# Kernel optimization log

Measured on AMD Instinct MI355X. Metric: run time of the kernel, lower is better.

Reference implementation:

```python
import jax, jax.numpy as jnp
import numpy as np

EMBED = 2048
HEADS = 16
NOPE = 128      # embed // heads
VDIM = 128
ROPE = 64
Q_HEAD = NOPE + ROPE  # 192
KV_RANK = 512
BASE = 10000.0


def _rope(x, offset=0):
    # x: [b, h, n, d] with d even; rotary (lrpe_type=1) on pair-interleaved dims
    d = x.shape[-1]
    n = x.shape[-2]
    theta = BASE ** (-2.0 * jnp.arange(d // 2, dtype=jnp.float32) / d)  # [d/2]
    pos = jnp.arange(n, dtype=jnp.float32) + offset                     # [n]
    ang = pos[:, None] * theta[None, :]                                  # [n, d/2]
    cos, sin = jnp.cos(ang), jnp.sin(ang)
    x1 = x[..., 0::2]
    x2 = x[..., 1::2]
    o1 = x1 * cos - x2 * sin
    o2 = x1 * sin + x2 * cos
    return jnp.stack([o1, o2], axis=-1).reshape(x.shape)


def setup_inputs() -> dict:
    key = jax.random.key(0)
    ks = jax.random.split(key, 6)
    b, n = 2, 2048
    s = lambda fin: 1.0 / np.sqrt(fin)
    return {
        "x": jax.random.normal(ks[0], (b, n, EMBED), jnp.float32),
        "Wqa": jax.random.normal(ks[1], (EMBED, 512), jnp.float32) * s(EMBED),
        "Wqb": jax.random.normal(ks[2], (512, HEADS * Q_HEAD), jnp.float32) * s(512),
        "Wkva": jax.random.normal(ks[3], (EMBED, KV_RANK + ROPE), jnp.float32) * s(EMBED),
        "Wkvb": jax.random.normal(ks[4], (KV_RANK, HEADS * (NOPE + VDIM)), jnp.float32) * s(KV_RANK),
        "Wout": jax.random.normal(ks[5], (HEADS * VDIM, EMBED), jnp.float32) * s(HEADS * VDIM),
    }


def reference(x, Wqa, Wqb, Wkva, Wkvb, Wout):
    b, n, _ = x.shape
    # low-rank Q projection
    q = (x @ Wqa) @ Wqb                                   # [b, n, h*192]
    q = q.reshape(b, n, HEADS, Q_HEAD).transpose(0, 2, 1, 3)  # [b, h, n, 192]
    q_nope, q_pe = q[..., :NOPE], q[..., NOPE:]
    # low-rank KV compression + shared rope key
    ckv = x @ Wkva                                        # [b, n, 512+64]
    compressed, k_pe = ckv[..., :KV_RANK], ckv[..., KV_RANK:]
    k_pe = jnp.broadcast_to(k_pe[:, None], (b, HEADS, n, ROPE))
    kv = compressed @ Wkvb                                # [b, n, h*(128+128)]
    kv = kv.reshape(b, n, HEADS, NOPE + VDIM).transpose(0, 2, 1, 3)
    k_nope, v = kv[..., :NOPE], kv[..., NOPE:]
    # partial RoPE on rope slice
    q_pe = _rope(q_pe)
    k_pe = _rope(k_pe)
    qf = jnp.concatenate([q_nope, q_pe], axis=-1)         # [b, h, n, 192]
    kf = jnp.concatenate([k_nope, k_pe], axis=-1)
    # causal SDPA, scale = 1/sqrt(q_head_dim)
    scale = 1.0 / np.sqrt(Q_HEAD)
    scores = jnp.einsum("bhnd,bhmd->bhnm", qf, kf) * scale
    causal = jnp.tril(jnp.ones((n, n), dtype=bool))
    scores = jnp.where(causal, scores, jnp.finfo(scores.dtype).min)
    attn = jax.nn.softmax(scores, axis=-1)
    out = jnp.einsum("bhnm,bhmd->bhnd", attn, v)          # [b, h, n, 128]
    out = out.transpose(0, 2, 1, 3).reshape(b, n, HEADS * VDIM)
    return out @ Wout
```

## Files before the change

### kernel.cpp

```cpp
#include <hip/hip_runtime.h>
#include <math.h>

typedef __bf16 bf16;
typedef __bf16 bf16x8 __attribute__((ext_vector_type(8)));
typedef float f32x4 __attribute__((ext_vector_type(4)));

#define HEADS 16
#define QHEAD 192
#define NB 2
#define SEQ 2048
#define ROWS (NB * SEQ)
#define QSCALE2 0.10411754584f
#define CSHIFT 11.5415603272f

__global__ __launch_bounds__(256) void prep(
    const float* __restrict__ x,
    const float* __restrict__ Wqa, const float* __restrict__ Wqb,
    const float* __restrict__ Wkva, const float* __restrict__ Wkvb,
    const float* __restrict__ Wout,
    bf16* __restrict__ xb,
    bf16* __restrict__ WfT, bf16* __restrict__ WqbT,
    bf16* __restrict__ WkvbT, bf16* __restrict__ WoutT)
{
    int t = blockIdx.x;
    if (t < 8192) {
        size_t i = ((size_t)t * 256 + threadIdx.x) * 4;
        float4 v = *(const float4*)(x + i);
        xb[i]     = (bf16)v.x;
        xb[i + 1] = (bf16)v.y;
        xb[i + 2] = (bf16)v.z;
        xb[i + 3] = (bf16)v.w;
        return;
    }
    t -= 8192;
    __shared__ float tile[32][33];
    const float* in; bf16* out; int R, C;
    if (t < 1024)      {            in = Wqa;  out = WfT;                      R = 2048; C = 512;  }
    else if (t < 2176) { t -= 1024; in = Wkva; out = WfT + (size_t)512 * 2048; R = 2048; C = 576;  }
    else if (t < 3712) { t -= 2176; in = Wqb;  out = WqbT;                     R = 512;  C = 3072; }
    else if (t < 5760) { t -= 3712; in = Wkvb; out = WkvbT;                    R = 512;  C = 4096; }
    else               { t -= 5760; in = Wout; out = WoutT;                    R = 2048; C = 2048; }
    int tilesX = (C + 31) >> 5;
    int bx = (t % tilesX) * 32, by = (t / tilesX) * 32;
    int tx = threadIdx.x & 31, ty = threadIdx.x >> 5;
    for (int i = 0; i < 32; i += 8) {
        int r = by + ty + i, c = bx + tx;
        tile[ty + i][tx] = (r < R && c < C) ? in[(size_t)r * C + c] : 0.f;
    }
    __syncthreads();
    for (int i = 0; i < 32; i += 8) {
        int c = bx + ty + i, r = by + tx;
        if (c < C && r < R) out[(size_t)c * R + r] = (bf16)tile[tx][ty + i];
    }
}

#define GEMM_BODY(Aptr, LDA, Bptr, LDB, KK, BNIDX)                              \
    __shared__ bf16 As[128 * 32];                                               \
    __shared__ bf16 Bs[128 * 32];                                               \
    const int tid  = threadIdx.x;                                               \
    const int wave = tid >> 6, lane = tid & 63;                                 \
    const int quad = lane >> 4, l16 = lane & 15;                                \
    const int bm = blockIdx.x * 128, bn = (BNIDX) * 128;                        \
    const int wm = (wave >> 1) * 64, wn = (wave & 1) * 64;                      \
    const int srow = lane >> 2, scol = (lane & 3) * 8;                          \
    f32x4 acc[4][4];                                                            \
    for (int i = 0; i < 4; i++)                                                 \
        for (int j = 0; j < 4; j++)                                             \
            acc[i][j] = (f32x4){0.f, 0.f, 0.f, 0.f};                            \
    for (int k0 = 0; k0 < (KK); k0 += 32) {                                     \
        _Pragma("unroll")                                                       \
        for (int s2 = 0; s2 < 2; s2++) {                                        \
            const int seg = wave * 2 + s2;                                      \
            const bf16* ga = (Aptr) + (size_t)(bm + seg * 16 + srow) * (LDA) + k0 + scol; \
            const bf16* gb = (Bptr) + (size_t)(bn + seg * 16 + srow) * (LDB) + k0 + scol; \
            __builtin_amdgcn_global_load_lds(                                   \
                (const __attribute__((address_space(1))) void*)ga,              \
                (__attribute__((address_space(3))) void*)&As[seg * 512], 16, 0, 0); \
            __builtin_amdgcn_global_load_lds(                                   \
                (const __attribute__((address_space(1))) void*)gb,              \
                (__attribute__((address_space(3))) void*)&Bs[seg * 512], 16, 0, 0); \
        }                                                                       \
        __syncthreads();                                                        \
        bf16x8 af[4], bfv[4];                                                   \
        for (int mi = 0; mi < 4; mi++)                                          \
            af[mi] = *(const bf16x8*)&As[(wm + mi * 16 + l16) * 32 + quad * 8]; \
        for (int ni = 0; ni < 4; ni++)                                          \
            bfv[ni] = *(const bf16x8*)&Bs[(wn + ni * 16 + l16) * 32 + quad * 8];\
        for (int mi = 0; mi < 4; mi++)                                          \
            for (int ni = 0; ni < 4; ni++)                                      \
                acc[mi][ni] = __builtin_amdgcn_mfma_f32_16x16x32_bf16(          \
                    af[mi], bfv[ni], acc[mi][ni], 0, 0, 0);                     \
        __syncthreads();                                                        \
    }

template <typename OutT>
__global__ __launch_bounds__(256) void gemm_bf16(
    const bf16* __restrict__ A, int lda,
    const bf16* __restrict__ Bt, int ldb,
    OutT* __restrict__ C, int ldc,
    int N, int K)
{
    GEMM_BODY(A, lda, Bt, ldb, K, blockIdx.y)
    for (int mi = 0; mi < 4; mi++)
        for (int ni = 0; ni < 4; ni++) {
            int col = bn + wn + ni * 16 + l16;
            if (col >= N) continue;
            int row0 = bm + wm + mi * 16 + quad * 4;
            for (int r = 0; r < 4; r++)
                C[(size_t)(row0 + r) * ldc + col] = (OutT)acc[mi][ni][r];
        }
}

__global__ __launch_bounds__(256) void gemm_qkv(
    const bf16* __restrict__ tc,
    const bf16* __restrict__ WqbT, const bf16* __restrict__ WkvbT,
    bf16* __restrict__ qf, bf16* __restrict__ kf, bf16* __restrict__ kvv)
{
    const int byAll = blockIdx.y;
    const bool isQ = byAll < 24;
    const bf16* A  = isQ ? tc : tc + 512;
    const bf16* Bt = isQ ? WqbT : WkvbT;
    const int bnIdx = isQ ? byAll : byAll - 24;
    GEMM_BODY(A, 1152, Bt, 512, 512, bnIdx)
    if (isQ) {
        const bool odd = l16 & 1;
        for (int mi = 0; mi < 4; mi++)
            for (int ni = 0; ni < 4; ni++) {
                int col0 = bn + wn + ni * 16;
                int h  = col0 / 192;
                int d0 = col0 - h * 192;
                int d  = d0 + l16;
                bool roped = d0 >= 128;
                float theta = 0.f;
                if (roped) theta = powf(10000.f, -(float)((d - 128) >> 1) / 32.f);
                for (int r = 0; r < 4; r++) {
                    int row = bm + wm + mi * 16 + quad * 4 + r;
                    int b = row >> 11, n = row & 2047;
                    float v = acc[mi][ni][r], res;
                    if (roped) {
                        float p = __shfl_xor(v, 1);
                        float sn, cs;
                        sincosf((float)n * theta, &sn, &cs);
                        float x1 = odd ? p : v, x2 = odd ? v : p;
                        res = odd ? (x1 * sn + x2 * cs) : (x1 * cs - x2 * sn);
                    } else res = v;
                    qf[(((size_t)(b * HEADS + h)) * SEQ + n) * QHEAD + d] =
                        (bf16)(res * QSCALE2);
                }
            }
    } else {
        for (int mi = 0; mi < 4; mi++)
            for (int ni = 0; ni < 4; ni++) {
                int col0 = bn + wn + ni * 16;
                int h  = col0 >> 8;
                int d0 = col0 & 255;
                int d  = d0 + l16;
                for (int r = 0; r < 4; r++) {
                    int row = bm + wm + mi * 16 + quad * 4 + r;
                    int b = row >> 11, n = row & 2047;
                    bf16 v = (bf16)acc[mi][ni][r];
                    if (d0 < 128)
                        kf[(((size_t)(b * HEADS + h)) * SEQ + n) * QHEAD + d] = v;
                    else
                        kvv[(size_t)row * 2048 + h * 128 + (d - 128)] = v;
                }
            }
    }
}

__global__ __launch_bounds__(256) void rope_vt(
    const bf16* __restrict__ tc, const bf16* __restrict__ kvv,
    bf16* __restrict__ kf, bf16* __restrict__ vT)
{
    int t = blockIdx.x;
    if (t < 8192) {
        __shared__ bf16 tile[32][33];
        int bh = t >> 8, rest = t & 255;
        int dv0 = (rest >> 6) * 32, nt0 = (rest & 63) * 32;
        int b = bh >> 4, h = bh & 15;
        int tx = threadIdx.x & 31, ty = threadIdx.x >> 5;
        for (int i = 0; i < 32; i += 8) {
            int n = nt0 + ty + i;
            tile[ty + i][tx] = kvv[((size_t)(b * SEQ + n)) * 2048 + h * 128 + dv0 + tx];
        }
        __syncthreads();
        for (int i = 0; i < 32; i += 8) {
            int dv = dv0 + ty + i;
            vT[((size_t)bh * 128 + dv) * SEQ + nt0 + tx] = tile[tx][ty + i];
        }
    } else {
        int gid = (t - 8192) * 256 + threadIdx.x;
        int row = gid >> 6, j = gid & 63;
        int b = row >> 11, n = row & 2047;
        int i = j >> 1;
        float x1 = (float)tc[(size_t)row * 1152 + 1024 + 2 * i];
        float x2 = (float)tc[(size_t)row * 1152 + 1024 + 2 * i + 1];
        float theta = powf(10000.f, -(float)i / 32.f);
        float sn, cs;
        sincosf((float)n * theta, &sn, &cs);
        bf16 rv = (bf16)((j & 1) ? (x1 * sn + x2 * cs) : (x1 * cs - x2 * sn));
        for (int h = 0; h < HEADS; h++)
            kf[(((size_t)(b * HEADS + h)) * SEQ + n) * QHEAD + 128 + j] = rv;
    }
}

__global__ __launch_bounds__(256) void attn_fa(
    const bf16* __restrict__ qf, const bf16* __restrict__ kf,
    const bf16* __restrict__ vT, bf16* __restrict__ attn_out)
{
    __shared__ bf16 Ks[64][200];
    __shared__ bf16 Vt[128][72];
    __shared__ bf16 Ps[4][16][72];

    const int bid = blockIdx.x;
    const int xcd = bid & 7, j = bid >> 3;
    const int qt = 31 - (j >> 2);
    const int bh = xcd + 8 * (j & 3);
    const int b = bh >> 4, h = bh & 15;
    const int tid  = threadIdx.x;
    const int wave = tid >> 6, lane = tid & 63;
    const int quad = lane >> 4, l16 = lane & 15;

    bf16x8 aq[6];
    {
        const bf16* qbase = qf + ((size_t)bh * SEQ + qt * 64 + wave * 16 + l16) * QHEAD;
        for (int ks = 0; ks < 6; ks++)
            aq[ks] = *(const bf16x8*)(qbase + ks * 32 + quad * 8);
    }
    f32x4 o[8];
    for (int i = 0; i < 8; i++) o[i] = (f32x4){0.f, 0.f, 0.f, 0.f};
    float lp[4] = {0.f, 0.f, 0.f, 0.f};

    for (int kt = 0; kt <= qt; kt++) {
#pragma unroll
        for (int i = 0; i < 6; i++) {
            int c = tid + i * 256;
            int r = c / 24, col = (c - r * 24) * 8;
            *(uint4*)&Ks[r][col] =
                *(const uint4*)(kf + ((size_t)bh * SEQ + kt * 64 + r) * QHEAD + col);
        }
#pragma unroll
        for (int i = 0; i < 4; i++) {
            int c = tid + i * 256;
            int dv = c >> 3, g = c & 7;
            *(uint4*)&Vt[dv][g * 8] =
                *(const uint4*)(vT + ((size_t)bh * 128 + dv) * SEQ + kt * 64 + g * 8);
        }
        __syncthreads();

        f32x4 sacc[4];
        for (int nt = 0; nt < 4; nt++) sacc[nt] = (f32x4){0.f, 0.f, 0.f, 0.f};
        for (int ks = 0; ks < 6; ks++)
            for (int nt = 0; nt < 4; nt++) {
                bf16x8 bk = *(const bf16x8*)&Ks[nt * 16 + l16][ks * 32 + quad * 8];
                sacc[nt] = __builtin_amdgcn_mfma_f32_16x16x32_bf16(aq[ks], bk, sacc[nt], 0, 0, 0);
            }

        const bool diag = (kt == qt);
#pragma unroll
        for (int r = 0; r < 4; r++) {
            const int qrow = wave * 16 + quad * 4 + r;
#pragma unroll
            for (int nt = 0; nt < 4; nt++) {
                float p;
                if (diag && (nt * 16 + l16 > qrow)) p = 0.f;
                else p = __builtin_amdgcn_exp2f(sacc[nt][r] - CSHIFT);
                lp[r] += p;
                Ps[wave][quad * 4 + r][nt * 16 + l16] = (bf16)p;
            }
        }
        __builtin_amdgcn_sched_barrier(0);

        for (int ks2 = 0; ks2 < 2; ks2++) {
            bf16x8 ap = *(const bf16x8*)&Ps[wave][l16][ks2 * 32 + quad * 8];
            for (int nv = 0; nv < 8; nv++) {
                bf16x8 bv = *(const bf16x8*)&Vt[nv * 16 + l16][ks2 * 32 + quad * 8];
                o[nv] = __builtin_amdgcn_mfma_f32_16x16x32_bf16(ap, bv, o[nv], 0, 0, 0);
            }
        }
        __syncthreads();
    }

#pragma unroll
    for (int r = 0; r < 4; r++) {
        lp[r] += __shfl_xor(lp[r], 8);
        lp[r] += __shfl_xor(lp[r], 4);
        lp[r] += __shfl_xor(lp[r], 2);
        lp[r] += __shfl_xor(lp[r], 1);
    }

    for (int r = 0; r < 4; r++) {
        float inv = 1.f / lp[r];
        size_t row = (size_t)b * SEQ + qt * 64 + wave * 16 + quad * 4 + r;
        for (int nv = 0; nv < 8; nv++)
            attn_out[row * 2048 + h * 128 + nv * 16 + l16] = (bf16)(o[nv][r] * inv);
    }
}

extern "C" void kernel_launch(void* const* d_in, const int* in_sizes, int n_in,
                              void* d_out, int out_size, void* d_ws, size_t ws_size,
                              hipStream_t stream)
{
    const float* x    = (const float*)d_in[0];
    const float* Wqa  = (const float*)d_in[1];
    const float* Wqb  = (const float*)d_in[2];
    const float* Wkva = (const float*)d_in[3];
    const float* Wkvb = (const float*)d_in[4];
    const float* Wout = (const float*)d_in[5];
    float* out = (float*)d_out;

    char* ws = (char*)d_ws;
    size_t off = 0;
    auto alloc = [&](size_t elems) { char* p = ws + off; off += elems * sizeof(bf16); return (bf16*)p; };
    bf16* xb    = alloc((size_t)ROWS * 2048);
    bf16* WfT   = alloc((size_t)1152 * 2048);
    bf16* WqbT  = alloc((size_t)3072 * 512);
    bf16* WkvbT = alloc((size_t)4096 * 512);
    bf16* WoutT = alloc((size_t)2048 * 2048);
    bf16* tc    = alloc((size_t)ROWS * 1152);
    bf16* kvv   = alloc((size_t)ROWS * 2048);
    bf16* vT    = alloc((size_t)32 * 128 * SEQ);
    bf16* qf    = alloc((size_t)32 * SEQ * QHEAD);
    bf16* kf    = alloc((size_t)32 * SEQ * QHEAD);
    bf16* attn  = xb;
    if (off > ws_size) return;

    dim3 blk(256);

    prep<<<dim3(18048), blk, 0, stream>>>(x, Wqa, Wqb, Wkva, Wkvb, Wout,
                                          xb, WfT, WqbT, WkvbT, WoutT);

    gemm_bf16<bf16><<<dim3(32, 9), blk, 0, stream>>>(xb, 2048, WfT, 2048, tc, 1152, 1088, 2048);

    gemm_qkv<<<dim3(32, 56), blk, 0, stream>>>(tc, WqbT, WkvbT, qf, kf, kvv);

    rope_vt<<<dim3(9216), blk, 0, stream>>>(tc, kvv, kf, vT);

    attn_fa<<<dim3(1024), blk, 0, stream>>>(qf, kf, vT, attn);

    gemm_bf16<float><<<dim3(32, 16), blk, 0, stream>>>(attn, 2048, WoutT, 2048, out, 2048, 2048, 2048);
}
```

Before: 417.7 us.

## Fuse V transpose into QKV GEMM epilogue, add rope table and narrow first GEMM

```diff
diff --git a/kernel.cpp b/kernel.cpp
--- a/kernel.cpp
+++ b/kernel.cpp
@@ -20,7 +20,8 @@
     const float* __restrict__ Wout,
     bf16* __restrict__ xb,
     bf16* __restrict__ WfT, bf16* __restrict__ WqbT,
-    bf16* __restrict__ WkvbT, bf16* __restrict__ WoutT)
+    bf16* __restrict__ WkvbT, bf16* __restrict__ WoutT,
+    float2* __restrict__ rope_tab)
 {
     int t = blockIdx.x;
     if (t < 8192) {
@@ -33,6 +34,15 @@
         return;
     }
     t -= 8192;
+    if (t >= 9856) {
+        int gid = (t - 9856) * 256 + threadIdx.x;
+        int n = gid >> 5, i = gid & 31;
+        float theta = powf(10000.f, -(float)i / 32.f);
+        float sn, cs;
+        sincosf((float)n * theta, &sn, &cs);
+        rope_tab[gid] = make_float2(cs, sn);
+        return;
+    }
     __shared__ float tile[32][33];
     const float* in; bf16* out; int R, C;
     if (t < 1024)      {            in = Wqa;  out = WfT;                      R = 2048; C = 512;  }
@@ -111,11 +121,63 @@
         }
 }
 
+__global__ __launch_bounds__(256) void gemm13_n64(
+    const bf16* __restrict__ A, const bf16* __restrict__ Bt,
+    bf16* __restrict__ tc)
+{
+    __shared__ bf16 As[128 * 32];
+    __shared__ bf16 Bs[64 * 32];
+    const int tid  = threadIdx.x;
+    const int wave = tid >> 6, lane = tid & 63;
+    const int quad = lane >> 4, l16 = lane & 15;
+    const int bm = blockIdx.x * 128, bn = blockIdx.y * 64;
+    const int srow = lane >> 2, scol = (lane & 3) * 8;
+    f32x4 acc[2][4];
+    for (int i = 0; i < 2; i++)
+        for (int j = 0; j < 4; j++) acc[i][j] = (f32x4){0.f, 0.f, 0.f, 0.f};
+    for (int k0 = 0; k0 < 2048; k0 += 32) {
+#pragma unroll
+        for (int s2 = 0; s2 < 2; s2++) {
+            const int seg = wave * 2 + s2;
+            const bf16* ga = A + (size_t)(bm + seg * 16 + srow) * 2048 + k0 + scol;
+            __builtin_amdgcn_global_load_lds(
+                (const __attribute__((address_space(1))) void*)ga,
+                (__attribute__((address_space(3))) void*)&As[seg * 512], 16, 0, 0);
+            if (s2 == 0) {
+                const bf16* gb = Bt + (size_t)(bn + wave * 16 + srow) * 2048 + k0 + scol;
+                __builtin_amdgcn_global_load_lds(
+                    (const __attribute__((address_space(1))) void*)gb,
+                    (__attribute__((address_space(3))) void*)&Bs[wave * 512], 16, 0, 0);
+            }
+        }
+        __syncthreads();
+        bf16x8 af[2], bfv[4];
+        for (int mi = 0; mi < 2; mi++)
+            af[mi] = *(const bf16x8*)&As[(wave * 32 + mi * 16 + l16) * 32 + quad * 8];
+        for (int ni = 0; ni < 4; ni++)
+            bfv[ni] = *(const bf16x8*)&Bs[(ni * 16 + l16) * 32 + quad * 8];
+        for (int mi = 0; mi < 2; mi++)
+            for (int ni = 0; ni < 4; ni++)
+                acc[mi][ni] = __builtin_amdgcn_mfma_f32_16x16x32_bf16(
+                    af[mi], bfv[ni], acc[mi][ni], 0, 0, 0);
+        __syncthreads();
+    }
+    for (int mi = 0; mi < 2; mi++)
+        for (int ni = 0; ni < 4; ni++) {
+            int col = bn + ni * 16 + l16;
+            int row0 = bm + wave * 32 + mi * 16 + quad * 4;
+            for (int r = 0; r < 4; r++)
+                tc[(size_t)(row0 + r) * 1152 + col] = (bf16)acc[mi][ni][r];
+        }
+}
+
 __global__ __launch_bounds__(256) void gemm_qkv(
     const bf16* __restrict__ tc,
     const bf16* __restrict__ WqbT, const bf16* __restrict__ WkvbT,
-    bf16* __restrict__ qf, bf16* __restrict__ kf, bf16* __restrict__ kvv)
-{
+    const float2* __restrict__ rope_tab,
+    bf16* __restrict__ qf, bf16* __restrict__ kf, bf16* __restrict__ vT)
+{
+    __shared__ bf16 Vs[64][132];
     const int byAll = blockIdx.y;
     const bool isQ = byAll < 24;
     const bf16* A  = isQ ? tc : tc + 512;
@@ -131,77 +193,79 @@
                 int d0 = col0 - h * 192;
                 int d  = d0 + l16;
                 bool roped = d0 >= 128;
-                float theta = 0.f;
-                if (roped) theta = powf(10000.f, -(float)((d - 128) >> 1) / 32.f);
+                int i = roped ? ((d - 128) >> 1) : 0;
                 for (int r = 0; r < 4; r++) {
                     int row = bm + wm + mi * 16 + quad * 4 + r;
                     int b = row >> 11, n = row & 2047;
                     float v = acc[mi][ni][r], res;
                     if (roped) {
                         float p = __shfl_xor(v, 1);
-                        float sn, cs;
-                        sincosf((float)n * theta, &sn, &cs);
+                        float2 cs = rope_tab[(n << 5) + i];
                         float x1 = odd ? p : v, x2 = odd ? v : p;
-                        res = odd ? (x1 * sn + x2 * cs) : (x1 * cs - x2 * sn);
+                        res = odd ? (x1 * cs.y + x2 * cs.x) : (x1 * cs.x - x2 * cs.y);
                     } else res = v;
                     qf[(((size_t)(b * HEADS + h)) * SEQ + n) * QHEAD + d] =
                         (bf16)(res * QSCALE2);
                 }
             }
-    } else {
+    } else if (!(bnIdx & 1)) {
+        const int h = bnIdx >> 1;
         for (int mi = 0; mi < 4; mi++)
             for (int ni = 0; ni < 4; ni++) {
-                int col0 = bn + wn + ni * 16;
-                int h  = col0 >> 8;
-                int d0 = col0 & 255;
-                int d  = d0 + l16;
+                int d = wn + ni * 16 + l16;
                 for (int r = 0; r < 4; r++) {
                     int row = bm + wm + mi * 16 + quad * 4 + r;
                     int b = row >> 11, n = row & 2047;
-                    bf16 v = (bf16)acc[mi][ni][r];
-                    if (d0 < 128)
-                        kf[(((size_t)(b * HEADS + h)) * SEQ + n) * QHEAD + d] = v;
-                    else
-                        kvv[(size_t)row * 2048 + h * 128 + (d - 128)] = v;
+                    kf[(((size_t)(b * HEADS + h)) * SEQ + n) * QHEAD + d] =
+                        (bf16)acc[mi][ni][r];
                 }
             }
-    }
-}
-
-__global__ __launch_bounds__(256) void rope_vt(
-    const bf16* __restrict__ tc, const bf16* __restrict__ kvv,
-    bf16* __restrict__ kf, bf16* __restrict__ vT)
-{
-    int t = blockIdx.x;
-    if (t < 8192) {
-        __shared__ bf16 tile[32][33];
-        int bh = t >> 8, rest = t & 255;
-        int dv0 = (rest >> 6) * 32, nt0 = (rest & 63) * 32;
-        int b = bh >> 4, h = bh & 15;
-        int tx = threadIdx.x & 31, ty = threadIdx.x >> 5;
-        for (int i = 0; i < 32; i += 8) {
-            int n = nt0 + ty + i;
-            tile[ty + i][tx] = kvv[((size_t)(b * SEQ + n)) * 2048 + h * 128 + dv0 + tx];
-        }
-        __syncthreads();
-        for (int i = 0; i < 32; i += 8) {
-            int dv = dv0 + ty + i;
-            vT[((size_t)bh * 128 + dv) * SEQ + nt0 + tx] = tile[tx][ty + i];
-        }
     } else {
-        int gid = (t - 8192) * 256 + threadIdx.x;
-        int row = gid >> 6, j = gid & 63;
-        int b = row >> 11, n = row & 2047;
-        int i = j >> 1;
-        float x1 = (float)tc[(size_t)row * 1152 + 1024 + 2 * i];
-        float x2 = (float)tc[(size_t)row * 1152 + 1024 + 2 * i + 1];
-        float theta = powf(10000.f, -(float)i / 32.f);
-        float sn, cs;
-        sincosf((float)n * theta, &sn, &cs);
-        bf16 rv = (bf16)((j & 1) ? (x1 * sn + x2 * cs) : (x1 * cs - x2 * sn));
-        for (int h = 0; h < HEADS; h++)
-            kf[(((size_t)(b * HEADS + h)) * SEQ + n) * QHEAD + 128 + j] = rv;
-    }
+        const int h = bnIdx >> 1;
+        const int bb = bm >> 11, n0 = bm & 2047;
+        const size_t vbase = (size_t)(bb * HEADS + h) * 128 * SEQ;
+#pragma unroll
+        for (int p = 0; p < 2; p++) {
+            if ((wave & 1) == p) {
+                for (int ni = 0; ni < 4; ni++)
+                    for (int mi = 0; mi < 4; mi++)
+                        for (int r = 0; r < 4; r++)
+                            Vs[ni * 16 + l16][wm + mi * 16 + quad * 4 + r] =
+                                (bf16)acc[mi][ni][r];
+            }
+            __syncthreads();
+            {
+                int dv_l = tid >> 2, seg = tid & 3;
+                const bf16* src = &Vs[dv_l][seg * 32];
+                bf16* dst = vT + vbase + (size_t)(p * 64 + dv_l) * SEQ + n0 + seg * 32;
+                uint4 v0 = *(const uint4*)(src);
+                uint4 v1 = *(const uint4*)(src + 8);
+                uint4 v2 = *(const uint4*)(src + 16);
+                uint4 v3 = *(const uint4*)(src + 24);
+                *(uint4*)(dst)      = v0;
+                *(uint4*)(dst + 8)  = v1;
+                *(uint4*)(dst + 16) = v2;
+                *(uint4*)(dst + 24) = v3;
+            }
+            __syncthreads();
+        }
+    }
+}
+
+__global__ __launch_bounds__(256) void rope_kpe(
+    const bf16* __restrict__ tc, const float2* __restrict__ rope_tab,
+    bf16* __restrict__ kf)
+{
+    int gid = blockIdx.x * 256 + threadIdx.x;
+    int row = gid >> 6, j = gid & 63;
+    int b = row >> 11, n = row & 2047;
+    int i = j >> 1;
+    float x1 = (float)tc[(size_t)row * 1152 + 1024 + 2 * i];
+    float x2 = (float)tc[(size_t)row * 1152 + 1024 + 2 * i + 1];
+    float2 cs = rope_tab[(n << 5) + i];
+    bf16 rv = (bf16)((j & 1) ? (x1 * cs.y + x2 * cs.x) : (x1 * cs.x - x2 * cs.y));
+    for (int h = 0; h < HEADS; h++)
+        kf[(((size_t)(b * HEADS + h)) * SEQ + n) * QHEAD + 128 + j] = rv;
 }
 
 __global__ __launch_bounds__(256) void attn_fa(
@@ -288,7 +352,6 @@
         lp[r] += __shfl_xor(lp[r], 2);
         lp[r] += __shfl_xor(lp[r], 1);
     }
-
     for (int r = 0; r < 4; r++) {
         float inv = 1.f / lp[r];
         size_t row = (size_t)b * SEQ + qt * 64 + wave * 16 + quad * 4 + r;
@@ -318,23 +381,23 @@
     bf16* WkvbT = alloc((size_t)4096 * 512);
     bf16* WoutT = alloc((size_t)2048 * 2048);
     bf16* tc    = alloc((size_t)ROWS * 1152);
-    bf16* kvv   = alloc((size_t)ROWS * 2048);
     bf16* vT    = alloc((size_t)32 * 128 * SEQ);
     bf16* qf    = alloc((size_t)32 * SEQ * QHEAD);
     bf16* kf    = alloc((size_t)32 * SEQ * QHEAD);
+    float2* rope_tab = (float2*)alloc((size_t)SEQ * 32 * 4);
     bf16* attn  = xb;
     if (off > ws_size) return;
 
     dim3 blk(256);
 
-    prep<<<dim3(18048), blk, 0, stream>>>(x, Wqa, Wqb, Wkva, Wkvb, Wout,
-                                          xb, WfT, WqbT, WkvbT, WoutT);
-
-    gemm_bf16<bf16><<<dim3(32, 9), blk, 0, stream>>>(xb, 2048, WfT, 2048, tc, 1152, 1088, 2048);
-
-    gemm_qkv<<<dim3(32, 56), blk, 0, stream>>>(tc, WqbT, WkvbT, qf, kf, kvv);
-
-    rope_vt<<<dim3(9216), blk, 0, stream>>>(tc, kvv, kf, vT);
+    prep<<<dim3(18304), blk, 0, stream>>>(x, Wqa, Wqb, Wkva, Wkvb, Wout,
+                                          xb, WfT, WqbT, WkvbT, WoutT, rope_tab);
+
+    gemm13_n64<<<dim3(32, 17), blk, 0, stream>>>(xb, WfT, tc);
+
+    gemm_qkv<<<dim3(32, 56), blk, 0, stream>>>(tc, WqbT, WkvbT, rope_tab, qf, kf, vT);
+
+    rope_kpe<<<dim3(1024), blk, 0, stream>>>(tc, rope_tab, kf);
 
     attn_fa<<<dim3(1024), blk, 0, stream>>>(qf, kf, vT, attn);
 
```

After: 589.9 us. 1.41x slower.
